# Kernel optimization log

Hardware: AMD Instinct MI355X
Metric: run time of the kernel (lower is better)

Reference implementation:

```python
import jax, jax.numpy as jnp
import numpy as np

B, T, S, H = 8, 128, 256, 512


def setup_inputs() -> dict:
    key = jax.random.key(0)
    ks = jax.random.split(key, 8)
    query = jax.random.normal(ks[0], (B, T, H), dtype=jnp.float32)
    encoder_outputs = jax.random.normal(ks[1], (B, S, H), dtype=jnp.float32)
    # lengths in [S//2, S], with max pinned to S (torch code requires lengths.max() == mask width == S)
    src_lengths = jax.random.randint(ks[2], (B,), S // 2, S + 1)
    src_lengths = src_lengths.at[0].set(S)
    scale = 1.0 / np.sqrt(H)
    W_s = jax.random.normal(ks[3], (H, H), dtype=jnp.float32) * scale
    W_h = jax.random.normal(ks[4], (H, H), dtype=jnp.float32) * scale
    v = jax.random.normal(ks[5], (H,), dtype=jnp.float32) * scale
    W_out = jax.random.normal(ks[6], (H, 2 * H), dtype=jnp.float32) * (1.0 / np.sqrt(2 * H))
    b_out = jax.random.normal(ks[7], (H,), dtype=jnp.float32) * 0.01
    return {"query": query, "encoder_outputs": encoder_outputs, "src_lengths": src_lengths,
            "W_s": W_s, "W_h": W_h, "v": v, "W_out": W_out, "b_out": b_out}


def reference(query, encoder_outputs, src_lengths, W_s, W_h, v, W_out, b_out):
    # Projections (torch Linear: x @ W.T)
    qs = jnp.einsum('bth,kh->btk', query, W_s)            # (B,T,H)
    hs = jnp.einsum('bsh,kh->bsk', encoder_outputs, W_h)  # (B,S,H)
    # Additive score: v . tanh(W_s q + W_h h) -> (B,T,S)
    scores = jnp.einsum('btsh,h->bts', jnp.tanh(qs[:, :, None, :] + hs[:, None, :, :]), v)
    mask = jnp.arange(scores.shape[-1])[None, :] < src_lengths[:, None]  # (B,S)
    scores = jnp.where(mask[:, None, :], scores, -jnp.inf)
    attn = jax.nn.softmax(scores, axis=-1)                # (B,T,S)
    context = jnp.einsum('bts,bsh->bth', attn, encoder_outputs)
    combined = jnp.concatenate([context, query], axis=-1)  # (B,T,2H)
    return jnp.tanh(jnp.einsum('btc,hc->bth', combined, W_out) + b_out)
```

## Files before the change

kernel.cpp:

```cpp
#include <hip/hip_runtime.h>

constexpr int B = 8, T = 128, S = 256, H = 512;

typedef __attribute__((ext_vector_type(4))) float f32x4;
typedef __attribute__((ext_vector_type(8))) float f32x8;
typedef __attribute__((ext_vector_type(8))) short short8;
typedef __attribute__((ext_vector_type(4))) short short4v;

#define DEVINL __device__ __forceinline__

DEVINL float bf2f(short s) {
  union { unsigned u; float f; } x;
  x.u = ((unsigned)(unsigned short)s) << 16;
  return x.f;
}
DEVINL short f2bf(float f) {
  unsigned u = __float_as_uint(f);
  return (short)((u + 0x7fffu + ((u >> 16) & 1u)) >> 16);
}
DEVINL float fast_tanh(float x) {
  float e = __builtin_amdgcn_exp2f(x * 2.8853900817779268f);
  return 1.0f - 2.0f * __builtin_amdgcn_rcpf(e + 1.0f);
}

constexpr float C2 = 2.8853900817779268f;
constexpr float L2E = 1.4426950408889634f;

constexpr size_t OFF_EH  = 0;
constexpr size_t OFF_PT  = OFF_EH + (size_t)B * H * S;
constexpr size_t OFF_ATT = OFF_PT + (size_t)B * H * S;
constexpr size_t OFF_QBF = OFF_ATT + (size_t)B * T * S;
constexpr size_t OFF_EBF = OFF_QBF + (size_t)B * T * H;
constexpr size_t OFF_WSB = OFF_EBF + (size_t)B * S * H;
constexpr size_t OFF_WHB = OFF_WSB + (size_t)H * H;
constexpr size_t OFF_WOB = OFF_WHB + (size_t)H * H;
constexpr size_t OFF_EQ  = OFF_WOB + (size_t)H * 2 * H;

__global__ __launch_bounds__(256) void prep_kernel(
    const float* __restrict__ q, const float* __restrict__ e,
    const float* __restrict__ ws, const float* __restrict__ wh,
    const float* __restrict__ wo, short* __restrict__ base) {
  int vi = blockIdx.x * 256 + threadIdx.x;
  if (vi >= 655360) return;
  const float* src; short* dst; int local; float scale;
  if (vi < 131072)      { src = q;  dst = base + OFF_QBF; local = vi;          scale = 1.f; }
  else if (vi < 393216) { src = e;  dst = base + OFF_EBF; local = vi - 131072; scale = 1.f; }
  else if (vi < 458752) { src = ws; dst = base + OFF_WSB; local = vi - 393216; scale = C2;  }
  else if (vi < 524288) { src = wh; dst = base + OFF_WHB; local = vi - 458752; scale = C2;  }
  else                  { src = wo; dst = base + OFF_WOB; local = vi - 524288; scale = 1.f; }
  float4 f = reinterpret_cast<const float4*>(src)[local];
  short4v o;
  o.x = f2bf(f.x * scale); o.y = f2bf(f.y * scale);
  o.z = f2bf(f.z * scale); o.w = f2bf(f.w * scale);
  *reinterpret_cast<short4v*>(dst + (size_t)local * 4) = o;
}

template <int MB, int NB>
DEVINL void gemm_tile_bf(const short* __restrict__ A, int lda,
                         const short* __restrict__ Wt, int ldw, int K,
                         int bm, int bn, short* As, short* Bs, f32x4* acc) {
  const int tid = threadIdx.x;
  const int lane = tid & 63;
  const int wm = (tid >> 6) >> 1, wn = (tid >> 6) & 1;
  const int g = lane >> 4, r = lane & 15;
  for (int k0 = 0; k0 < K; k0 += 64) {
    __syncthreads();
#pragma unroll
    for (int p = 0; p < MB; ++p) {
      const int idx = p * 256 + tid;
      const int row = idx >> 3, c = idx & 7;
      short8 av = *reinterpret_cast<const short8*>(&A[(size_t)(bm + row) * lda + k0 + c * 8]);
      *reinterpret_cast<short8*>(&As[row * 64 + ((c ^ (row & 7)) * 8)]) = av;
    }
#pragma unroll
    for (int p = 0; p < NB; ++p) {
      const int idx = p * 256 + tid;
      const int row = idx >> 3, c = idx & 7;
      short8 wv = *reinterpret_cast<const short8*>(&Wt[(size_t)(bn + row) * ldw + k0 + c * 8]);
      *reinterpret_cast<short8*>(&Bs[row * 64 + ((c ^ (row & 7)) * 8)]) = wv;
    }
    __syncthreads();
#pragma unroll
    for (int kc = 0; kc < 2; ++kc) {
      short8 af[MB], bfr[NB];
#pragma unroll
      for (int mb = 0; mb < MB; ++mb) {
        const int ra = wm * (MB * 16) + mb * 16 + r;
        af[mb] = *reinterpret_cast<const short8*>(&As[ra * 64 + (((kc * 4 + g) ^ (r & 7)) * 8)]);
      }
#pragma unroll
      for (int nb = 0; nb < NB; ++nb) {
        const int rb = wn * (NB * 16) + nb * 16 + r;
        bfr[nb] = *reinterpret_cast<const short8*>(&Bs[rb * 64 + (((kc * 4 + g) ^ (r & 7)) * 8)]);
      }
#pragma unroll
      for (int mb = 0; mb < MB; ++mb)
#pragma unroll
        for (int nb = 0; nb < NB; ++nb)
          acc[mb * NB + nb] =
              __builtin_amdgcn_mfma_f32_16x16x32_bf16(af[mb], bfr[nb], acc[mb * NB + nb], 0, 0, 0);
    }
  }
}

__global__ __launch_bounds__(256) void proj_kernel(short* __restrict__ wsbase,
                                                   float* __restrict__ eq) {
  __shared__ short As[64 * 64], Bs[64 * 64];
  f32x4 acc[4];
#pragma unroll
  for (int i = 0; i < 4; ++i) acc[i] = (f32x4){0.f, 0.f, 0.f, 0.f};
  int bid = blockIdx.x;
  int mode; const short* A; const short* W; int ldw;
  const short* q_bf = wsbase + OFF_QBF;
  const short* e_bf = wsbase + OFF_EBF;
  if (bid < 128)      { mode = 0; A = q_bf; W = wsbase + OFF_WSB; ldw = H; }
  else if (bid < 384) { mode = 1; bid -= 128; A = e_bf; W = wsbase + OFF_WHB; ldw = H; }
  else                { mode = 2; bid -= 384; A = e_bf; W = wsbase + OFF_WOB; ldw = 2 * H; }
  const int bm = (bid >> 3) * 64, bn = (bid & 7) * 64;
  gemm_tile_bf<2, 2>(A, H, W, ldw, H, bm, bn, As, Bs, acc);

  short* eh_p = wsbase + OFF_EH;
  short* P_t = wsbase + OFF_PT;
  const int lane = threadIdx.x & 63, wave = threadIdx.x >> 6;
  const int wm = wave >> 1, wn = wave & 1, g = lane >> 4, r = lane & 15;
#pragma unroll
  for (int mb = 0; mb < 2; ++mb)
#pragma unroll
    for (int nb = 0; nb < 2; ++nb) {
      const f32x4 a4 = acc[mb * 2 + nb];
      const int m0 = bm + wm * 32 + mb * 16 + g * 4;
      const int col = bn + wn * 32 + nb * 16 + r;
      if (mode == 0) {
#pragma unroll
        for (int i = 0; i < 4; ++i)
          eq[(size_t)(m0 + i) * H + col] = __builtin_amdgcn_exp2f(a4[i]);
      } else if (mode == 1) {
        const int bb = m0 >> 8, sl = m0 & 255;
        const size_t base = ((size_t)(bb * (H / 8) + (col >> 3)) * S + sl) * 8 + (col & 7);
#pragma unroll
        for (int i = 0; i < 4; ++i)
          eh_p[base + (size_t)i * 8] = f2bf(__builtin_amdgcn_exp2f(a4[i]));
      } else {
        const int bb = m0 >> 8, sl = m0 & 255;
        short4v o;
        o.x = f2bf(a4[0]); o.y = f2bf(a4[1]); o.z = f2bf(a4[2]); o.w = f2bf(a4[3]);
        *reinterpret_cast<short4v*>(&P_t[((size_t)bb * H + col) * S + sl]) = o;
      }
    }
}

__global__ __launch_bounds__(1024, 8) void attn_kernel(
    const float* __restrict__ eq, const short* __restrict__ eh_p,
    const float* __restrict__ v, const int* __restrict__ lens,
    short* __restrict__ attn_bf) {
  __shared__ float s_part[4][2][S];
  __shared__ float red_m[2][4], red_s[2][4];
  const int tid = threadIdx.x, lane = tid & 63;
  const int wu = __builtin_amdgcn_readfirstlane(tid >> 6);
  const int sg = wu & 3, qtr = wu >> 2;
  const int b = blockIdx.x >> 6;
  const int t0 = (blockIdx.x & 63) * 2;
  const int s = sg * 64 + lane;

  const float* qp = eq + (size_t)(b * T + t0) * H + qtr * (H / 4);
  const float* vp = v + qtr * (H / 4);
  const short8* ep = reinterpret_cast<const short8*>(eh_p) +
                     ((size_t)(b * (H / 8) + qtr * (H / 32)) * S + s);

  float acc0 = 0.f, acc1 = 0.f;
  short8 e0 = ep[0], e1 = ep[(size_t)S];
  for (int it = 0; it < 8; ++it) {
    const size_t ne = (it < 7) ? (size_t)(2 * it + 2) * S : 0;
    const short8 e0n = ep[ne], e1n = ep[ne + S];
    const int h = it * 16;
    float ef[16];
#pragma unroll
    for (int j = 0; j < 8; ++j) { ef[j] = bf2f(e0[j]); ef[8 + j] = bf2f(e1[j]); }
    const f32x8 vA = *reinterpret_cast<const f32x8*>(vp + h);
    const f32x8 vB = *reinterpret_cast<const f32x8*>(vp + h + 8);
#pragma unroll
    for (int tt = 0; tt < 2; ++tt) {
      const float* qq = qp + (size_t)tt * H + h;
      const f32x8 qA = *reinterpret_cast<const f32x8*>(qq);
      const f32x8 qB = *reinterpret_cast<const f32x8*>(qq + 8);
      float a = 0.f;
#pragma unroll
      for (int j = 0; j < 8; j += 2) {
        const float Aa = fmaf(qA[j], ef[j], 1.0f);
        const float Bb = fmaf(qA[j + 1], ef[j + 1], 1.0f);
        const float rr = __builtin_amdgcn_rcpf(Aa * Bb);
        a = fmaf(fmaf(vA[j + 1], Aa, vA[j] * Bb), rr, a);
      }
#pragma unroll
      for (int j = 0; j < 8; j += 2) {
        const float Aa = fmaf(qB[j], ef[8 + j], 1.0f);
        const float Bb = fmaf(qB[j + 1], ef[8 + j + 1], 1.0f);
        const float rr = __builtin_amdgcn_rcpf(Aa * Bb);
        a = fmaf(fmaf(vB[j + 1], Aa, vB[j] * Bb), rr, a);
      }
      if (tt == 0) acc0 += a; else acc1 += a;
    }
    e0 = e0n; e1 = e1n;
  }
  s_part[qtr][0][s] = acc0;
  s_part[qtr][1][s] = acc1;
  __syncthreads();

  const int len = lens[b];
  const float a0 = s_part[0][0][s] + s_part[1][0][s] + s_part[2][0][s] + s_part[3][0][s];
  const float a1 = s_part[0][1][s] + s_part[1][1][s] + s_part[2][1][s] + s_part[3][1][s];
  const float y0 = (s < len) ? (-2.0f * L2E * a0) : -1e30f;
  const float y1 = (s < len) ? (-2.0f * L2E * a1) : -1e30f;
  float m0 = y0, m1 = y1;
#pragma unroll
  for (int off = 32; off > 0; off >>= 1) {
    m0 = fmaxf(m0, __shfl_xor(m0, off));
    m1 = fmaxf(m1, __shfl_xor(m1, off));
  }
  if (qtr == 0 && lane == 0) { red_m[0][sg] = m0; red_m[1][sg] = m1; }
  __syncthreads();
  const float mt0 = fmaxf(fmaxf(red_m[0][0], red_m[0][1]), fmaxf(red_m[0][2], red_m[0][3]));
  const float mt1 = fmaxf(fmaxf(red_m[1][0], red_m[1][1]), fmaxf(red_m[1][2], red_m[1][3]));
  const float p0 = __builtin_amdgcn_exp2f(y0 - mt0);
  const float p1 = __builtin_amdgcn_exp2f(y1 - mt1);
  float u0 = p0, u1 = p1;
#pragma unroll
  for (int off = 32; off > 0; off >>= 1) {
    u0 += __shfl_xor(u0, off);
    u1 += __shfl_xor(u1, off);
  }
  if (qtr == 0 && lane == 0) { red_s[0][sg] = u0; red_s[1][sg] = u1; }
  __syncthreads();
  if (qtr == 0) {
    const float tot0 = red_s[0][0] + red_s[0][1] + red_s[0][2] + red_s[0][3];
    const float tot1 = red_s[1][0] + red_s[1][1] + red_s[1][2] + red_s[1][3];
    attn_bf[(size_t)(b * T + t0) * S + s] = f2bf(p0 * __builtin_amdgcn_rcpf(tot0));
    attn_bf[(size_t)(b * T + t0 + 1) * S + s] = f2bf(p1 * __builtin_amdgcn_rcpf(tot1));
  }
}

__global__ __launch_bounds__(256) void out_kernel(
    const short* __restrict__ wsbase, const float* __restrict__ bias,
    float* __restrict__ out) {
  __shared__ short As[32 * 64], Bs[64 * 64];
  f32x4 acc[2];
#pragma unroll
  for (int i = 0; i < 2; ++i) acc[i] = (f32x4){0.f, 0.f, 0.f, 0.f};
  const int bm = (blockIdx.x >> 3) * 32, bn = (blockIdx.x & 7) * 64;
  const int batch = bm >> 7;
  const short* attn_bf = wsbase + OFF_ATT;
  const short* P_t = wsbase + OFF_PT;
  const short* q_bf = wsbase + OFF_QBF;
  const short* Wob = wsbase + OFF_WOB;
  gemm_tile_bf<1, 2>(attn_bf, S, P_t + (size_t)batch * H * S, S, S, bm, bn, As, Bs, acc);
  gemm_tile_bf<1, 2>(q_bf, H, Wob + H, 2 * H, H, bm, bn, As, Bs, acc);
  const int lane = threadIdx.x & 63, wave = threadIdx.x >> 6;
  const int wm = wave >> 1, wn = wave & 1, g = lane >> 4, r = lane & 15;
#pragma unroll
  for (int nb = 0; nb < 2; ++nb) {
    const f32x4 a4 = acc[nb];
    const int col = bn + wn * 32 + nb * 16 + r;
    const float bb = bias[col];
#pragma unroll
    for (int i = 0; i < 4; ++i) {
      const int row = bm + wm * 16 + g * 4 + i;
      out[(size_t)row * H + col] = fast_tanh(a4[i] + bb);
    }
  }
}

extern "C" void kernel_launch(void* const* d_in, const int* in_sizes, int n_in,
                              void* d_out, int out_size, void* d_ws, size_t ws_size,
                              hipStream_t stream) {
  const float* query = (const float*)d_in[0];
  const float* enc = (const float*)d_in[1];
  const int* lens = (const int*)d_in[2];
  const float* W_s = (const float*)d_in[3];
  const float* W_h = (const float*)d_in[4];
  const float* v = (const float*)d_in[5];
  const float* W_out = (const float*)d_in[6];
  const float* b_out = (const float*)d_in[7];
  float* out = (float*)d_out;

  short* wsb = (short*)d_ws;
  short* eh_p = wsb + OFF_EH;
  short* attn_bf = wsb + OFF_ATT;
  float* eq = (float*)(wsb + OFF_EQ);

  prep_kernel<<<2560, 256, 0, stream>>>(query, enc, W_s, W_h, W_out, wsb);
  proj_kernel<<<640, 256, 0, stream>>>(wsb, eq);
  attn_kernel<<<B * T / 2, 1024, 0, stream>>>(eq, eh_p, v, lens, attn_bf);
  out_kernel<<<256, 256, 0, stream>>>(wsb, b_out, out);
}
```

Measured before the change: 45.05 us.

## Move query-side output GEMM into projection kernel and unroll attention loads

```diff
diff --git a/kernel.cpp b/kernel.cpp
--- a/kernel.cpp
+++ b/kernel.cpp
@@ -35,6 +35,7 @@
 constexpr size_t OFF_WHB = OFF_WSB + (size_t)H * H;
 constexpr size_t OFF_WOB = OFF_WHB + (size_t)H * H;
 constexpr size_t OFF_EQ  = OFF_WOB + (size_t)H * 2 * H;
+constexpr size_t OFF_R   = OFF_EQ + (size_t)2 * B * T * H;
 
 __global__ __launch_bounds__(256) void prep_kernel(
     const float* __restrict__ q, const float* __restrict__ e,
@@ -104,7 +105,9 @@
 }
 
 __global__ __launch_bounds__(256) void proj_kernel(short* __restrict__ wsbase,
-                                                   float* __restrict__ eq) {
+                                                   const float* __restrict__ bias,
+                                                   float* __restrict__ eq,
+                                                   float* __restrict__ R) {
   __shared__ short As[64 * 64], Bs[64 * 64];
   f32x4 acc[4];
 #pragma unroll
@@ -115,7 +118,8 @@
   const short* e_bf = wsbase + OFF_EBF;
   if (bid < 128)      { mode = 0; A = q_bf; W = wsbase + OFF_WSB; ldw = H; }
   else if (bid < 384) { mode = 1; bid -= 128; A = e_bf; W = wsbase + OFF_WHB; ldw = H; }
-  else                { mode = 2; bid -= 384; A = e_bf; W = wsbase + OFF_WOB; ldw = 2 * H; }
+  else if (bid < 640) { mode = 2; bid -= 384; A = e_bf; W = wsbase + OFF_WOB; ldw = 2 * H; }
+  else                { mode = 3; bid -= 640; A = q_bf; W = wsbase + OFF_WOB + H; ldw = 2 * H; }
   const int bm = (bid >> 3) * 64, bn = (bid & 7) * 64;
   gemm_tile_bf<2, 2>(A, H, W, ldw, H, bm, bn, As, Bs, acc);
 
@@ -140,11 +144,16 @@
 #pragma unroll
         for (int i = 0; i < 4; ++i)
           eh_p[base + (size_t)i * 8] = f2bf(__builtin_amdgcn_exp2f(a4[i]));
-      } else {
+      } else if (mode == 2) {
         const int bb = m0 >> 8, sl = m0 & 255;
         short4v o;
         o.x = f2bf(a4[0]); o.y = f2bf(a4[1]); o.z = f2bf(a4[2]); o.w = f2bf(a4[3]);
         *reinterpret_cast<short4v*>(&P_t[((size_t)bb * H + col) * S + sl]) = o;
+      } else {
+        const float bb = bias[col];
+#pragma unroll
+        for (int i = 0; i < 4; ++i)
+          R[(size_t)(m0 + i) * H + col] = a4[i] + bb;
       }
     }
 }
@@ -168,10 +177,10 @@
                      ((size_t)(b * (H / 8) + qtr * (H / 32)) * S + s);
 
   float acc0 = 0.f, acc1 = 0.f;
-  short8 e0 = ep[0], e1 = ep[(size_t)S];
+#pragma unroll
   for (int it = 0; it < 8; ++it) {
-    const size_t ne = (it < 7) ? (size_t)(2 * it + 2) * S : 0;
-    const short8 e0n = ep[ne], e1n = ep[ne + S];
+    const short8 e0 = ep[(size_t)(2 * it) * S];
+    const short8 e1 = ep[(size_t)(2 * it + 1) * S];
     const int h = it * 16;
     float ef[16];
 #pragma unroll
@@ -200,7 +209,6 @@
       }
       if (tt == 0) acc0 += a; else acc1 += a;
     }
-    e0 = e0n; e1 = e1n;
   }
   s_part[qtr][0][s] = acc0;
   s_part[qtr][1][s] = acc1;
@@ -240,7 +248,7 @@
 }
 
 __global__ __launch_bounds__(256) void out_kernel(
-    const short* __restrict__ wsbase, const float* __restrict__ bias,
+    const short* __restrict__ wsbase, const float* __restrict__ R,
     float* __restrict__ out) {
   __shared__ short As[32 * 64], Bs[64 * 64];
   f32x4 acc[2];
@@ -250,21 +258,17 @@
   const int batch = bm >> 7;
   const short* attn_bf = wsbase + OFF_ATT;
   const short* P_t = wsbase + OFF_PT;
-  const short* q_bf = wsbase + OFF_QBF;
-  const short* Wob = wsbase + OFF_WOB;
   gemm_tile_bf<1, 2>(attn_bf, S, P_t + (size_t)batch * H * S, S, S, bm, bn, As, Bs, acc);
-  gemm_tile_bf<1, 2>(q_bf, H, Wob + H, 2 * H, H, bm, bn, As, Bs, acc);
   const int lane = threadIdx.x & 63, wave = threadIdx.x >> 6;
   const int wm = wave >> 1, wn = wave & 1, g = lane >> 4, r = lane & 15;
 #pragma unroll
   for (int nb = 0; nb < 2; ++nb) {
     const f32x4 a4 = acc[nb];
     const int col = bn + wn * 32 + nb * 16 + r;
-    const float bb = bias[col];
 #pragma unroll
     for (int i = 0; i < 4; ++i) {
       const int row = bm + wm * 16 + g * 4 + i;
-      out[(size_t)row * H + col] = fast_tanh(a4[i] + bb);
+      out[(size_t)row * H + col] = fast_tanh(a4[i] + R[(size_t)row * H + col]);
     }
   }
 }
@@ -286,9 +290,10 @@
   short* eh_p = wsb + OFF_EH;
   short* attn_bf = wsb + OFF_ATT;
   float* eq = (float*)(wsb + OFF_EQ);
+  float* R = (float*)(wsb + OFF_R);
 
   prep_kernel<<<2560, 256, 0, stream>>>(query, enc, W_s, W_h, W_out, wsb);
-  proj_kernel<<<640, 256, 0, stream>>>(wsb, eq);
+  proj_kernel<<<768, 256, 0, stream>>>(wsb, b_out, eq, R);
   attn_kernel<<<B * T / 2, 1024, 0, stream>>>(eq, eh_p, v, lens, attn_bf);
-  out_kernel<<<256, 256, 0, stream>>>(wsb, b_out, out);
-}
+  out_kernel<<<256, 256, 0, stream>>>(wsb, R, out);
+}
```

New measurement: 49.07 us. 1.09x slower.
